# Performance work log

Measured on AMD Instinct MI355X. Metric: run time of the kernel, lower is better.

## Reference

```python
import jax, jax.numpy as jnp
import numpy as np

CONF_THRES = 0.4
IOU_THRES = 0.45
MAX_WH = 4096.0   # class offset for non-agnostic NMS (torch code: max_wh)
K_PRE = 1024      # candidates kept for the O(K^2) NMS stage (<= max_nms=30000)
MAX_DET = 300     # max detections per image (torch default)
B, N, NC = 16, 25200, 80


def xywh2xyxy(x):
    xy, wh = x[..., :2], x[..., 2:4]
    return jnp.concatenate([xy - wh * 0.5, xy + wh * 0.5], axis=-1)


def box_iou(a, b):
    # a: [K,4], b: [K,4] in xyxy
    area_a = (a[:, 2] - a[:, 0]) * (a[:, 3] - a[:, 1])
    area_b = (b[:, 2] - b[:, 0]) * (b[:, 3] - b[:, 1])
    lt = jnp.maximum(a[:, None, :2], b[None, :, :2])
    rb = jnp.minimum(a[:, None, 2:], b[None, :, 2:])
    inter = jnp.clip(rb - lt, 0.0, None).prod(-1)
    return inter / (area_a[:, None] + area_b[None, :] - inter + 1e-7)


def _nms_single(pred, conf_logit, logit, head):
    # pred [N,85] (decoded, sigmoided), conf_logit [N,5] raw, logit [N,80] raw, head [N]
    xc = pred[:, 4] > CONF_THRES                      # objectness gate
    obj_sig = jax.nn.sigmoid(conf_logit[:, 4:5])      # [N,1]
    log_sig = jax.nn.sigmoid(logit) * obj_sig         # sel_prob == 'objclass'
    cls_scores = pred[:, 5:] * pred[:, 4:5]           # x[:,5:] *= x[:,4:5]
    box = xywh2xyxy(pred[:, :4])                      # [N,4]
    conf = cls_scores.max(axis=1)                     # best class conf
    j = cls_scores.argmax(axis=1).astype(pred.dtype)  # best class id
    valid = xc & (conf > CONF_THRES)
    score = jnp.where(valid, conf, 0.0)
    # top-K candidates (sorted descending) -> fixed-shape NMS
    top_s, top_i = jax.lax.top_k(score, K_PRE)
    valid_k = top_s > 0.0
    boxes_k = box[top_i] + j[top_i, None] * MAX_WH    # per-class box offset (agnostic=False)
    iou = box_iou(boxes_k, boxes_k)                   # [K,K]
    idx = jnp.arange(K_PRE)

    def body(i, keep):
        sup = (iou[i] > IOU_THRES) & (idx > i) & keep[i]
        return keep & ~sup

    keep = jax.lax.fori_loop(0, K_PRE, body, valid_k)
    final_score = jnp.where(keep, top_s, 0.0)
    _, sel = jax.lax.top_k(final_score, MAX_DET)      # first MAX_DET survivors
    gi = top_i[sel]
    m = (final_score[sel] > 0.0).astype(pred.dtype)[:, None]  # validity mask
    det = jnp.concatenate([box[gi], conf[gi, None], j[gi, None]], axis=1)  # [300,6] xyxy,conf,cls
    # pack: det(6) | class logits*obj(80) | obj_conf(1) | classHead(1) | valid(1) -> [300,89]
    return jnp.concatenate(
        [det * m, log_sig[gi] * m, obj_sig[gi] * m, head[gi, None] * m, m], axis=1)


def setup_inputs() -> dict:
    key = jax.random.key(0)
    k1, k2, k3, k4, k5, k6 = jax.random.split(key, 6)
    xy = jax.random.uniform(k1, (B, N, 2), jnp.float32) * 640.0
    wh = 2.0 + jax.random.uniform(k2, (B, N, 2), jnp.float32) * 198.0
    objcls = jax.random.uniform(k3, (B, N, 1 + NC), jnp.float32)
    prediction = jnp.concatenate([xy, wh, objcls], axis=-1)       # [B,N,85]
    pred_conf_logits = jax.random.normal(k4, (B, N, 5), jnp.float32)
    logits = jax.random.normal(k5, (B, N, NC), jnp.float32)
    class_head = jax.random.randint(k6, (B, N), 0, 3).astype(jnp.float32)
    return {"prediction": prediction, "pred_conf_logits": pred_conf_logits,
            "logits": logits, "class_head": class_head}


def reference(prediction, pred_conf_logits, logits, class_head):
    return jax.vmap(_nms_single)(prediction, pred_conf_logits, logits, class_head)
```

## Files before the change

kernel.cpp:

```cpp
#include <hip/hip_runtime.h>
#include <math.h>

#define BATCH 16
#define NN 25200
#define NCLS 80
#define K_PRE 1024
#define MAX_DET 300
#define CONF_T 0.4f
#define IOU_T 0.45f
#define TBIAS 0x3E000000u
#define RROWS 128
#define STHREADS 512
#define CAND_STRIDE 50400

__global__ void __launch_bounds__(STHREADS) score_kernel(
    const float* __restrict__ pred, unsigned long long* __restrict__ keys,
    unsigned* __restrict__ ghist) {
    __shared__ float srow[RROWS * 85];
    __shared__ unsigned lh[1024];

    const int tile = blockIdx.x, b = blockIdx.y, tid = threadIdx.x;
    const int row0 = tile * RROWS;
    int nrows = NN - row0;
    if (nrows > RROWS) nrows = RROWS;

    const float4* g4 = (const float4*)(pred + ((size_t)b * NN + row0) * 85);
    float4* l4 = (float4*)srow;
    const int nf4 = (nrows * 85) >> 2;
    for (int i = tid; i < nf4; i += STHREADS) l4[i] = g4[i];
    lh[tid] = 0u;
    lh[tid + STHREADS] = 0u;
    __syncthreads();

    const int r = tid >> 2, sub = tid & 3;
    float best = 0.0f;
    int bc = sub * 20;
    float obj = 0.0f;
    if (r < nrows) {
        obj = srow[r * 85 + 4];
        if (obj > CONF_T) {
            const float* cp = &srow[r * 85 + 5 + sub * 20];
#pragma unroll
            for (int i = 0; i < 20; ++i) {
                float v = cp[i] * obj;
                if (v > best) { best = v; bc = sub * 20 + i; }
            }
        }
    }
#pragma unroll
    for (int d = 1; d < 4; d <<= 1) {
        float ov = __shfl_xor(best, d);
        int oc = __shfl_xor(bc, d);
        if (ov > best || (ov == best && oc < bc)) { best = ov; bc = oc; }
    }
    if (r < nrows && sub == 0) {
        unsigned t = (obj > CONF_T && best > CONF_T)
                         ? (__float_as_uint(best) - TBIAS) : 0u;
        int n = row0 + r;
        keys[(size_t)b * NN + n] =
            ((unsigned long long)t << 22) |
            ((unsigned long long)(unsigned)(NN - 1 - n) << 7) | (unsigned)bc;
        if (t) atomicAdd(&lh[t >> 15], 1u);
    }
    __syncthreads();
    for (int i = tid; i < 1024; i += STHREADS) {
        unsigned v = lh[i];
        if (v) atomicAdd(&ghist[b * 1024 + i], v);
    }
}

__global__ void __launch_bounds__(1024) topk_kernel(
    const unsigned long long* __restrict__ keys,
    const unsigned* __restrict__ ghist, const float* __restrict__ pred,
    float* __restrict__ ws_f) {
    __shared__ unsigned sA[1024], sB[1024];
    __shared__ unsigned long long skeys[2048];
    __shared__ unsigned sel_d0, sel_cnt;

    const int b = blockIdx.x, tid = threadIdx.x;
    const unsigned long long* bk = keys + (size_t)b * NN;

    unsigned* src = sA;
    unsigned* dst = sB;
    src[tid] = ghist[b * 1024 + tid];
    __syncthreads();
    for (int off = 1; off < 1024; off <<= 1) {
        dst[tid] = src[tid] + ((tid + off < 1024) ? src[tid + off] : 0u);
        __syncthreads();
        unsigned* t2 = src; src = dst; dst = t2;
    }
    unsigned total = src[0];
    unsigned K = total < 1024u ? total : 1024u;
    if (tid == 0) { sel_d0 = 0u; sel_cnt = 0u; }
    skeys[tid] = 0ull;
    skeys[tid + 1024] = 0ull;
    __syncthreads();
    if (total) {
        unsigned geq = src[tid];
        unsigned gt = (tid < 1023) ? src[tid + 1] : 0u;
        if (gt < K && K <= geq) sel_d0 = (unsigned)tid;
    }
    __syncthreads();
    const unsigned d0 = sel_d0;

    for (int base = 0; base < 25600; base += 1024) {
        int i = base + tid;
        if (i < NN) {
            unsigned long long key = bk[i];
            unsigned t = (unsigned)(key >> 22);
            if (t && (t >> 15) >= d0) {
                unsigned p = atomicAdd(&sel_cnt, 1u);
                if (p < 2048u) skeys[p] = key;
            }
        }
    }
    __syncthreads();

    for (unsigned k2 = 2; k2 <= 2048; k2 <<= 1) {
        for (unsigned j = k2 >> 1; j > 0; j >>= 1) {
            unsigned i = ((tid & ~(j - 1)) << 1) | (tid & (j - 1));
            unsigned ixj = i | j;
            unsigned long long a = skeys[i], c = skeys[ixj];
            bool desc = ((i & k2) == 0u);
            if (desc ? (a < c) : (a > c)) { skeys[i] = c; skeys[ixj] = a; }
            __syncthreads();
        }
    }

    unsigned long long key = skeys[tid];
    unsigned t = (unsigned)(key >> 22);
    int n = NN - 1 - (int)((key >> 7) & 32767u);
    float* cbase = ws_f + (size_t)b * CAND_STRIDE;
    float* cx0 = cbase;
    float* cy0 = cbase + 1024;
    float* cx1 = cbase + 2048;
    float* cy1 = cbase + 3072;
    float* carea = cbase + 4096;
    float* cscore = cbase + 5120;
    int* ccls = (int*)(cbase + 6144);
    int* cgi = (int*)(cbase + 7168);
    int* keep = (int*)(cbase + 8192);
    keep[tid] = 0;
    cgi[tid] = n;
    if (t == 0u) {
        ccls[tid] = 255;
    } else {
        const float* row = pred + ((size_t)b * NN + n) * 85;
        float x = row[0], y = row[1], w = row[2], h = row[3];
        float bx0 = x - w * 0.5f, by0 = y - h * 0.5f;
        float bx1 = x + w * 0.5f, by1 = y + h * 0.5f;
        cx0[tid] = bx0; cy0[tid] = by0; cx1[tid] = bx1; cy1[tid] = by1;
        carea[tid] = (bx1 - bx0) * (by1 - by0);
        cscore[tid] = __uint_as_float(t + TBIAS);
        ccls[tid] = (int)(key & 127u);
    }
}

__global__ void __launch_bounds__(64) nms_kernel(float* __restrict__ ws_f) {
    __shared__ int mlist[K_PRE];
    __shared__ float bx0[K_PRE], by0[K_PRE], bx1[K_PRE], by1[K_PRE],
        bar[K_PRE];
    __shared__ unsigned char kf[K_PRE];

    const int b = blockIdx.x / NCLS, c = blockIdx.x % NCLS;
    const int lane = threadIdx.x;
    float* cbase = ws_f + (size_t)b * CAND_STRIDE;
    const float* cx0 = cbase;
    const float* cy0 = cbase + 1024;
    const float* cx1 = cbase + 2048;
    const float* cy1 = cbase + 3072;
    const float* carea = cbase + 4096;
    const int* ccls = (const int*)(cbase + 6144);
    int* keep = (int*)(cbase + 8192);

    int m = 0;
    for (int w = 0; w < K_PRE / 64; ++w) {
        int i = w * 64 + lane;
        bool my = (ccls[i] == c);
        unsigned long long bal = __ballot(my);
        if (my) {
            int pos = __popcll(bal & ((1ull << lane) - 1ull));
            mlist[m + pos] = i;
        }
        m += __popcll(bal);
    }
    for (int j = lane; j < m; j += 64) {
        int i = mlist[j];
        bx0[j] = cx0[i]; by0[j] = cy0[i];
        bx1[j] = cx1[i]; by1[j] = cy1[i];
        bar[j] = carea[i];
        kf[j] = 1;
    }
    __syncthreads();

    for (int i = 0; i < m; ++i) {
        if (kf[i]) {
            float ax0 = bx0[i], ay0 = by0[i], ax1 = bx1[i], ay1 = by1[i];
            float aa = bar[i];
            for (int j = i + 1 + lane; j < m; j += 64) {
                if (kf[j]) {
                    float lx = fmaxf(ax0, bx0[j]);
                    float ly = fmaxf(ay0, by0[j]);
                    float rx = fminf(ax1, bx1[j]);
                    float ry = fminf(ay1, by1[j]);
                    float iw = fmaxf(rx - lx, 0.0f);
                    float ih = fmaxf(ry - ly, 0.0f);
                    float inter = iw * ih;
                    float iou = inter / (aa + bar[j] - inter + 1e-7f);
                    if (iou > IOU_T) kf[j] = 0;
                }
            }
        }
        __syncthreads();
    }
    for (int j = lane; j < m; j += 64)
        if (kf[j]) keep[mlist[j]] = 1;
}

__global__ void __launch_bounds__(1024) output_kernel(
    const float* __restrict__ conf_logits, const float* __restrict__ logits,
    const float* __restrict__ head, const float* __restrict__ ws_f,
    float* __restrict__ out) {
    __shared__ unsigned sA[1024], sB[1024];
    const int b = blockIdx.x, tid = threadIdx.x;
    const float* cbase = ws_f + (size_t)b * CAND_STRIDE;
    const float* cx0 = cbase;
    const float* cy0 = cbase + 1024;
    const float* cx1 = cbase + 2048;
    const float* cy1 = cbase + 3072;
    const float* cscore = cbase + 5120;
    const int* ccls = (const int*)(cbase + 6144);
    const int* cgi = (const int*)(cbase + 7168);
    const int* keep = (const int*)(cbase + 8192);

    int kp = keep[tid];
    unsigned* src = sA;
    unsigned* dst = sB;
    src[tid] = (unsigned)kp;
    __syncthreads();
    for (int off = 1; off < 1024; off <<= 1) {
        dst[tid] = src[tid] + ((tid >= off) ? src[tid - off] : 0u);
        __syncthreads();
        unsigned* t2 = src; src = dst; dst = t2;
    }
    int rank = (int)src[tid] - kp;

    if (kp && rank < MAX_DET) {
        int gi = cgi[tid];
        float* orow = out + ((size_t)b * MAX_DET + rank) * 89;
        orow[0] = cx0[tid]; orow[1] = cy0[tid];
        orow[2] = cx1[tid]; orow[3] = cy1[tid];
        orow[4] = cscore[tid];
        orow[5] = (float)ccls[tid];
        float cl = conf_logits[((size_t)b * NN + gi) * 5 + 4];
        float obj_sig = 1.0f / (1.0f + expf(-cl));
        const float4* lrow4 =
            (const float4*)(logits + ((size_t)b * NN + gi) * NCLS);
#pragma unroll 4
        for (int q = 0; q < 20; ++q) {
            float4 l4 = lrow4[q];
            orow[6 + 4 * q + 0] = obj_sig / (1.0f + expf(-l4.x));
            orow[6 + 4 * q + 1] = obj_sig / (1.0f + expf(-l4.y));
            orow[6 + 4 * q + 2] = obj_sig / (1.0f + expf(-l4.z));
            orow[6 + 4 * q + 3] = obj_sig / (1.0f + expf(-l4.w));
        }
        orow[86] = obj_sig;
        orow[87] = head[(size_t)b * NN + gi];
        orow[88] = 1.0f;
    }
}

extern "C" void kernel_launch(void* const* d_in, const int* in_sizes, int n_in,
                              void* d_out, int out_size, void* d_ws,
                              size_t ws_size, hipStream_t stream) {
    const float* pred        = (const float*)d_in[0];
    const float* conf_logits = (const float*)d_in[1];
    const float* logits      = (const float*)d_in[2];
    const float* head        = (const float*)d_in[3];
    float* out = (float*)d_out;

    char* ws = (char*)d_ws;
    unsigned long long* keys = (unsigned long long*)ws;
    unsigned* ghist = (unsigned*)(ws + (size_t)BATCH * NN * 8);
    float* ws_f = (float*)ws;

    hipMemsetAsync(d_out, 0, (size_t)out_size * sizeof(float), stream);
    hipMemsetAsync(ghist, 0, (size_t)BATCH * 1024 * sizeof(unsigned), stream);

    dim3 sgrid((NN + RROWS - 1) / RROWS, BATCH);
    score_kernel<<<sgrid, STHREADS, 0, stream>>>(pred, keys, ghist);
    topk_kernel<<<BATCH, 1024, 0, stream>>>(keys, ghist, pred, ws_f);
    nms_kernel<<<BATCH * NCLS, 64, 0, stream>>>(ws_f);
    output_kernel<<<BATCH, 1024, 0, stream>>>(conf_logits, logits, head, ws_f,
                                              out);
}
```

Baseline: 333.3 us.

## Fuse top-k, per-class NMS and output into one kernel per image

Merges the top-k selection, the per-class NMS and the output packing into a single block-per-image kernel that keeps candidate boxes in shared memory instead of a global workspace. The histogram moves from global atomics in the score kernel into a shared-memory pass over the keys. NMS now runs with one wavefront per class, using bitmask alive-sets and a shuffle-min to pick the next kept box. Both memsets are removed by zeroing only the unused output rows. This cuts launch count and global round-trips, at the cost of using only 16 blocks for the histogram and NMS work.

```diff
diff --git a/kernel.cpp b/kernel.cpp
--- a/kernel.cpp
+++ b/kernel.cpp
@@ -11,13 +11,10 @@
 #define TBIAS 0x3E000000u
 #define RROWS 128
 #define STHREADS 512
-#define CAND_STRIDE 50400
 
 __global__ void __launch_bounds__(STHREADS) score_kernel(
-    const float* __restrict__ pred, unsigned long long* __restrict__ keys,
-    unsigned* __restrict__ ghist) {
+    const float* __restrict__ pred, unsigned long long* __restrict__ keys) {
     __shared__ float srow[RROWS * 85];
-    __shared__ unsigned lh[1024];
 
     const int tile = blockIdx.x, b = blockIdx.y, tid = threadIdx.x;
     const int row0 = tile * RROWS;
@@ -28,8 +25,6 @@
     float4* l4 = (float4*)srow;
     const int nf4 = (nrows * 85) >> 2;
     for (int i = tid; i < nf4; i += STHREADS) l4[i] = g4[i];
-    lh[tid] = 0u;
-    lh[tid + STHREADS] = 0u;
     __syncthreads();
 
     const int r = tid >> 2, sub = tid & 3;
@@ -60,30 +55,41 @@
         keys[(size_t)b * NN + n] =
             ((unsigned long long)t << 22) |
             ((unsigned long long)(unsigned)(NN - 1 - n) << 7) | (unsigned)bc;
-        if (t) atomicAdd(&lh[t >> 15], 1u);
-    }
-    __syncthreads();
-    for (int i = tid; i < 1024; i += STHREADS) {
-        unsigned v = lh[i];
-        if (v) atomicAdd(&ghist[b * 1024 + i], v);
     }
 }
 
-__global__ void __launch_bounds__(1024) topk_kernel(
+__global__ void __launch_bounds__(1024) fused_kernel(
     const unsigned long long* __restrict__ keys,
-    const unsigned* __restrict__ ghist, const float* __restrict__ pred,
-    float* __restrict__ ws_f) {
+    const float* __restrict__ pred,
+    const float* __restrict__ conf_logits,
+    const float* __restrict__ logits,
+    const float* __restrict__ head,
+    float* __restrict__ out) {
     __shared__ unsigned sA[1024], sB[1024];
     __shared__ unsigned long long skeys[2048];
+    __shared__ float bx0[K_PRE], by0[K_PRE], bx1[K_PRE], by1[K_PRE],
+        bar_[K_PRE], bsc[K_PRE];
+    __shared__ unsigned char bcls[K_PRE];
+    __shared__ unsigned short bgi[K_PRE];
+    __shared__ unsigned char bkeep[K_PRE];
     __shared__ unsigned sel_d0, sel_cnt;
 
     const int b = blockIdx.x, tid = threadIdx.x;
     const unsigned long long* bk = keys + (size_t)b * NN;
 
+    sA[tid] = 0u;
+    __syncthreads();
+    for (int base = 0; base < 25600; base += 1024) {
+        int i = base + tid;
+        if (i < NN) {
+            unsigned t = (unsigned)(bk[i] >> 22);
+            if (t) atomicAdd(&sA[t >> 15], 1u);
+        }
+    }
+    __syncthreads();
+
     unsigned* src = sA;
     unsigned* dst = sB;
-    src[tid] = ghist[b * 1024 + tid];
-    __syncthreads();
     for (int off = 1; off < 1024; off <<= 1) {
         dst[tid] = src[tid] + ((tid + off < 1024) ? src[tid + off] : 0u);
         __syncthreads();
@@ -127,78 +133,62 @@
         }
     }
 
-    unsigned long long key = skeys[tid];
-    unsigned t = (unsigned)(key >> 22);
-    int n = NN - 1 - (int)((key >> 7) & 32767u);
-    float* cbase = ws_f + (size_t)b * CAND_STRIDE;
-    float* cx0 = cbase;
-    float* cy0 = cbase + 1024;
-    float* cx1 = cbase + 2048;
-    float* cy1 = cbase + 3072;
-    float* carea = cbase + 4096;
-    float* cscore = cbase + 5120;
-    int* ccls = (int*)(cbase + 6144);
-    int* cgi = (int*)(cbase + 7168);
-    int* keep = (int*)(cbase + 8192);
-    keep[tid] = 0;
-    cgi[tid] = n;
-    if (t == 0u) {
-        ccls[tid] = 255;
-    } else {
-        const float* row = pred + ((size_t)b * NN + n) * 85;
-        float x = row[0], y = row[1], w = row[2], h = row[3];
-        float bx0 = x - w * 0.5f, by0 = y - h * 0.5f;
-        float bx1 = x + w * 0.5f, by1 = y + h * 0.5f;
-        cx0[tid] = bx0; cy0[tid] = by0; cx1[tid] = bx1; cy1[tid] = by1;
-        carea[tid] = (bx1 - bx0) * (by1 - by0);
-        cscore[tid] = __uint_as_float(t + TBIAS);
-        ccls[tid] = (int)(key & 127u);
-    }
-}
-
-__global__ void __launch_bounds__(64) nms_kernel(float* __restrict__ ws_f) {
-    __shared__ int mlist[K_PRE];
-    __shared__ float bx0[K_PRE], by0[K_PRE], bx1[K_PRE], by1[K_PRE],
-        bar[K_PRE];
-    __shared__ unsigned char kf[K_PRE];
-
-    const int b = blockIdx.x / NCLS, c = blockIdx.x % NCLS;
-    const int lane = threadIdx.x;
-    float* cbase = ws_f + (size_t)b * CAND_STRIDE;
-    const float* cx0 = cbase;
-    const float* cy0 = cbase + 1024;
-    const float* cx1 = cbase + 2048;
-    const float* cy1 = cbase + 3072;
-    const float* carea = cbase + 4096;
-    const int* ccls = (const int*)(cbase + 6144);
-    int* keep = (int*)(cbase + 8192);
-
-    int m = 0;
-    for (int w = 0; w < K_PRE / 64; ++w) {
-        int i = w * 64 + lane;
-        bool my = (ccls[i] == c);
-        unsigned long long bal = __ballot(my);
-        if (my) {
-            int pos = __popcll(bal & ((1ull << lane) - 1ull));
-            mlist[m + pos] = i;
-        }
-        m += __popcll(bal);
-    }
-    for (int j = lane; j < m; j += 64) {
-        int i = mlist[j];
-        bx0[j] = cx0[i]; by0[j] = cy0[i];
-        bx1[j] = cx1[i]; by1[j] = cy1[i];
-        bar[j] = carea[i];
-        kf[j] = 1;
-    }
-    __syncthreads();
-
-    for (int i = 0; i < m; ++i) {
-        if (kf[i]) {
-            float ax0 = bx0[i], ay0 = by0[i], ax1 = bx1[i], ay1 = by1[i];
-            float aa = bar[i];
-            for (int j = i + 1 + lane; j < m; j += 64) {
-                if (kf[j]) {
+    {
+        unsigned long long key = skeys[tid];
+        unsigned t = (unsigned)(key >> 22);
+        int n = NN - 1 - (int)((key >> 7) & 32767u);
+        bkeep[tid] = 0;
+        bgi[tid] = (unsigned short)n;
+        if (t == 0u) {
+            bcls[tid] = 255;
+            bsc[tid] = 0.0f;
+        } else {
+            const float* row = pred + ((size_t)b * NN + n) * 85;
+            float x = row[0], y = row[1], w = row[2], h = row[3];
+            float vx0 = x - w * 0.5f, vy0 = y - h * 0.5f;
+            float vx1 = x + w * 0.5f, vy1 = y + h * 0.5f;
+            bx0[tid] = vx0; by0[tid] = vy0; bx1[tid] = vx1; by1[tid] = vy1;
+            bar_[tid] = (vx1 - vx0) * (vy1 - vy0);
+            bsc[tid] = __uint_as_float(t + TBIAS);
+            bcls[tid] = (unsigned char)(key & 127u);
+        }
+    }
+    __syncthreads();
+
+    {
+        const int lane = tid & 63;
+        const int wv = tid >> 6;
+        unsigned char myc[16];
+#pragma unroll
+        for (int k = 0; k < 16; ++k) myc[k] = bcls[(k << 6) | lane];
+
+        for (int ci = 0; ci < 5; ++ci) {
+            const int c = wv + (ci << 4);
+            unsigned alive = 0u;
+#pragma unroll
+            for (int k = 0; k < 16; ++k)
+                if (myc[k] == (unsigned char)c) alive |= (1u << k);
+            unsigned keptm = 0u;
+            for (;;) {
+                int s = alive ? ((__builtin_ctz(alive) << 6) | lane)
+                              : (1 << 30);
+#pragma unroll
+                for (int d = 32; d; d >>= 1) {
+                    int o = __shfl_xor(s, d);
+                    s = o < s ? o : s;
+                }
+                if (s >= (1 << 30)) break;
+                if ((s & 63) == lane) {
+                    alive &= ~(1u << (s >> 6));
+                    keptm |= (1u << (s >> 6));
+                }
+                float ax0 = bx0[s], ay0 = by0[s], ax1 = bx1[s], ay1 = by1[s];
+                float aa = bar_[s];
+                unsigned rem = alive;
+                while (rem) {
+                    int k = __builtin_ctz(rem);
+                    rem &= rem - 1;
+                    int j = (k << 6) | lane;
                     float lx = fmaxf(ax0, bx0[j]);
                     float ly = fmaxf(ay0, by0[j]);
                     float rx = fminf(ax1, bx1[j]);
@@ -206,36 +196,21 @@
                     float iw = fmaxf(rx - lx, 0.0f);
                     float ih = fmaxf(ry - ly, 0.0f);
                     float inter = iw * ih;
-                    float iou = inter / (aa + bar[j] - inter + 1e-7f);
-                    if (iou > IOU_T) kf[j] = 0;
+                    float iou = inter / (aa + bar_[j] - inter + 1e-7f);
+                    if (iou > IOU_T) alive &= ~(1u << k);
                 }
             }
-        }
-        __syncthreads();
-    }
-    for (int j = lane; j < m; j += 64)
-        if (kf[j]) keep[mlist[j]] = 1;
-}
-
-__global__ void __launch_bounds__(1024) output_kernel(
-    const float* __restrict__ conf_logits, const float* __restrict__ logits,
-    const float* __restrict__ head, const float* __restrict__ ws_f,
-    float* __restrict__ out) {
-    __shared__ unsigned sA[1024], sB[1024];
-    const int b = blockIdx.x, tid = threadIdx.x;
-    const float* cbase = ws_f + (size_t)b * CAND_STRIDE;
-    const float* cx0 = cbase;
-    const float* cy0 = cbase + 1024;
-    const float* cx1 = cbase + 2048;
-    const float* cy1 = cbase + 3072;
-    const float* cscore = cbase + 5120;
-    const int* ccls = (const int*)(cbase + 6144);
-    const int* cgi = (const int*)(cbase + 7168);
-    const int* keep = (const int*)(cbase + 8192);
-
-    int kp = keep[tid];
-    unsigned* src = sA;
-    unsigned* dst = sB;
+            while (keptm) {
+                int k = __builtin_ctz(keptm);
+                keptm &= keptm - 1;
+                bkeep[(k << 6) | lane] = 1;
+            }
+        }
+    }
+    __syncthreads();
+
+    int kp = (int)bkeep[tid];
+    src = sA; dst = sB;
     src[tid] = (unsigned)kp;
     __syncthreads();
     for (int off = 1; off < 1024; off <<= 1) {
@@ -244,14 +219,15 @@
         unsigned* t2 = src; src = dst; dst = t2;
     }
     int rank = (int)src[tid] - kp;
+    int kcnt = (int)src[1023];
 
     if (kp && rank < MAX_DET) {
-        int gi = cgi[tid];
+        int gi = (int)bgi[tid];
         float* orow = out + ((size_t)b * MAX_DET + rank) * 89;
-        orow[0] = cx0[tid]; orow[1] = cy0[tid];
-        orow[2] = cx1[tid]; orow[3] = cy1[tid];
-        orow[4] = cscore[tid];
-        orow[5] = (float)ccls[tid];
+        orow[0] = bx0[tid]; orow[1] = by0[tid];
+        orow[2] = bx1[tid]; orow[3] = by1[tid];
+        orow[4] = bsc[tid];
+        orow[5] = (float)bcls[tid];
         float cl = conf_logits[((size_t)b * NN + gi) * 5 + 4];
         float obj_sig = 1.0f / (1.0f + expf(-cl));
         const float4* lrow4 =
@@ -268,6 +244,11 @@
         orow[87] = head[(size_t)b * NN + gi];
         orow[88] = 1.0f;
     }
+    if (tid < MAX_DET && tid >= kcnt) {
+        float* orow = out + ((size_t)b * MAX_DET + tid) * 89;
+#pragma unroll
+        for (int q = 0; q < 89; ++q) orow[q] = 0.0f;
+    }
 }
 
 extern "C" void kernel_launch(void* const* d_in, const int* in_sizes, int n_in,
@@ -279,18 +260,10 @@
     const float* head        = (const float*)d_in[3];
     float* out = (float*)d_out;
 
-    char* ws = (char*)d_ws;
-    unsigned long long* keys = (unsigned long long*)ws;
-    unsigned* ghist = (unsigned*)(ws + (size_t)BATCH * NN * 8);
-    float* ws_f = (float*)ws;
-
-    hipMemsetAsync(d_out, 0, (size_t)out_size * sizeof(float), stream);
-    hipMemsetAsync(ghist, 0, (size_t)BATCH * 1024 * sizeof(unsigned), stream);
+    unsigned long long* keys = (unsigned long long*)d_ws;
 
     dim3 sgrid((NN + RROWS - 1) / RROWS, BATCH);
-    score_kernel<<<sgrid, STHREADS, 0, stream>>>(pred, keys, ghist);
-    topk_kernel<<<BATCH, 1024, 0, stream>>>(keys, ghist, pred, ws_f);
-    nms_kernel<<<BATCH * NCLS, 64, 0, stream>>>(ws_f);
-    output_kernel<<<BATCH, 1024, 0, stream>>>(conf_logits, logits, head, ws_f,
-                                              out);
+    score_kernel<<<sgrid, STHREADS, 0, stream>>>(pred, keys);
+    fused_kernel<<<BATCH, 1024, 0, stream>>>(keys, pred, conf_logits, logits,
+                                             head, out);
 }
```

Measured after the change: 359.6 us. +7.9%, slower.
